# Optimization experiments

Measured on AMD Instinct MI355X. Metric: run time of the kernel, lower is better.

Reference implementation:

```python
import jax, jax.numpy as jnp
import numpy as np

B = 128          # batch
M_SIZE = 32      # mps bond dimension (init kwarg mps_size)
NQ = 16          # num_qubits -> 2**16 basis states


def setup_inputs() -> dict:
    key = jax.random.key(0)
    ks = jax.random.split(key, 4)
    def lin(k, out_d, in_d):
        return jax.random.normal(k, (out_d, in_d), jnp.float32) * (1.0 / np.sqrt(in_d))
    mat = M_SIZE * M_SIZE
    return {
        "x": jax.random.normal(ks[0], (B, 4), jnp.float32),
        "W1": lin(ks[1], 1024, 4),        "b1": jnp.zeros((1024,), jnp.float32),
        "W2": lin(ks[2], 32, 1024),       "b2": jnp.zeros((32,), jnp.float32),
        "W3": lin(ks[3], 2 * mat, 32),    "b3": jnp.zeros((2 * mat,), jnp.float32),
        "num_qubits": NQ,
    }


def _chain_products(M, k):
    """M: [2, B, m, m] site matrices (index 0 = spin_up, 1 = spin_down).
    Returns [2**k, B, m, m]: matrix products A_{s1} @ ... @ A_{sk} for every
    length-k bit string s, ordered as ascending binary (MSB = first/leftmost site),
    matching seq_gen's enumeration order."""
    arr = M
    for _ in range(k - 1):  # recursive doubling over sites (static small loop)
        arr = jnp.einsum('sbij,tbjk->stbik', arr, M)
        arr = arr.reshape((-1,) + M.shape[1:])
    return arr


def reference(x, W1, b1, W2, b2, W3, b3, num_qubits):
    # Encoder MLP (dropout is identity in eval mode)
    h = jax.nn.relu(x @ W1.T + b1)
    h = jax.nn.relu(h @ W2.T + b2)
    e = h @ W3.T + b3                         # [B, 2*m*m]
    m = int(np.sqrt(e.shape[-1] // 2))
    # view(-1, 2, m, m); split dim=1 -> spin_up = [:,0], spin_down = [:,1]
    Ms = e.reshape(-1, 2, m, m).transpose(1, 0, 2, 3)   # [2, B, m, m]
    # Decode: coeff(state) = trace(prod of site matrices). Split the chain in
    # two halves; trace(L_s @ R_t) = sum_ij L[s,i,j] * R[t,j,i].
    k1 = num_qubits // 2
    k2 = num_qubits - k1
    L = _chain_products(Ms, k1)               # [2^k1, B, m, m]
    R = _chain_products(Ms, k2)               # [2^k2, B, m, m]
    coeffs = jnp.einsum('sbij,tbji->stb', L, R)   # [2^k1, 2^k2, B]
    gs = coeffs.reshape(-1, coeffs.shape[-1]).T   # [B, 2^n], binary-ascending order
    return gs / jnp.linalg.norm(gs, axis=1, keepdims=True)
```

## Files before the change

### kernel.cpp

```cpp
#include <hip/hip_runtime.h>
#include <hip/hip_bf16.h>
#include <math.h>

#define BDIM 128

typedef short sh8 __attribute__((ext_vector_type(8)));
typedef __bf16 bf8 __attribute__((ext_vector_type(8)));
typedef float f32x4 __attribute__((ext_vector_type(4)));

__device__ inline float bf2f(unsigned short u) {
    union { unsigned int i; float f; } v; v.i = ((unsigned int)u) << 16; return v.f;
}
__device__ inline unsigned short f2bf(float f) {
    union { unsigned int i; float f; } v; v.f = f;
    unsigned int x = v.i;
    return (unsigned short)((x + 0x7FFFu + ((x >> 16) & 1u)) >> 16);
}

__device__ inline sh8 xshuf(sh8 v, int u) {
    switch (u & 7) {
    case 0: return v;
    case 1: return __builtin_shufflevector(v,v,1,0,3,2,5,4,7,6);
    case 2: return __builtin_shufflevector(v,v,2,3,0,1,6,7,4,5);
    case 3: return __builtin_shufflevector(v,v,3,2,1,0,7,6,5,4);
    case 4: return __builtin_shufflevector(v,v,4,5,6,7,0,1,2,3);
    case 5: return __builtin_shufflevector(v,v,5,4,7,6,1,0,3,2);
    case 6: return __builtin_shufflevector(v,v,6,7,4,5,2,3,0,1);
    default: return __builtin_shufflevector(v,v,7,6,5,4,3,2,1,0);
    }
}

__global__ __launch_bounds__(256) void enc_fused(
    const float* __restrict__ x,
    const float* __restrict__ W1, const float* __restrict__ b1,
    const float* __restrict__ W2, const float* __restrict__ b2,
    const float* __restrict__ W3, const float* __restrict__ b3,
    unsigned short* __restrict__ P4n, unsigned short* __restrict__ P4t,
    float* __restrict__ nrm)
{
    __shared__ float h1[1024];
    __shared__ float part[8][33];
    __shared__ float h2[32];
    __shared__ float aT[2][32][36], an[2][32][36];
    __shared__ float p2T[4][32][36], p2n[4][32][36];
    int b = blockIdx.x, t = threadIdx.x;
    if (t == 0) nrm[b] = 0.f;
    float x0 = x[b*4+0], x1 = x[b*4+1], x2 = x[b*4+2], x3 = x[b*4+3];
#pragma unroll
    for (int q = 0; q < 4; ++q) {
        int j = t + 256*q;
        float4 w = *(const float4*)(W1 + (size_t)j*4);
        float v = x0*w.x + x1*w.y + x2*w.z + x3*w.w + b1[j];
        h1[j] = v > 0.f ? v : 0.f;
    }
    __syncthreads();
    {
        int o = t & 31, chunk = t >> 5;
        const float* w2r = W2 + (size_t)o*1024 + chunk*128;
        const float* h1r = h1 + chunk*128;
        float s = 0.f;
#pragma unroll
        for (int k = 0; k < 128; k += 4) {
            float4 w = *(const float4*)(w2r + k);
            s += h1r[k]*w.x + h1r[k+1]*w.y + h1r[k+2]*w.z + h1r[k+3]*w.w;
        }
        part[chunk][o] = s;
    }
    __syncthreads();
    if (t < 32) {
        float s = b2[t];
#pragma unroll
        for (int c = 0; c < 8; ++c) s += part[c][t];
        h2[t] = s > 0.f ? s : 0.f;
    }
    __syncthreads();
#pragma unroll
    for (int q = 0; q < 8; ++q) {
        int j = t + 256*q;
        const float* w3r = W3 + (size_t)j*32;
        float s = b3[j];
#pragma unroll
        for (int i = 0; i < 32; i += 4) {
            float4 w = *(const float4*)(w3r + i);
            s += h2[i]*w.x + h2[i+1]*w.y + h2[i+2]*w.z + h2[i+3]*w.w;
        }
        int spin = j >> 10, off = j & 1023;
        int row = off >> 5, c = off & 31;
        an[spin][row][c] = s;
        aT[spin][c][row] = s;
    }
    __syncthreads();
    int w = t >> 6, l = t & 63;
    int r0 = (l >> 3) << 2, c0 = (l & 7) << 2;
    {
        float acc[4][4] = {};
#pragma unroll 8
        for (int kk = 0; kk < 32; ++kk) {
            float a[4], bb[4];
            *(float4*)a  = *(const float4*)&aT[w>>1][kk][r0];
            *(float4*)bb = *(const float4*)&an[w&1][kk][c0];
#pragma unroll
            for (int i = 0; i < 4; ++i)
#pragma unroll
                for (int j = 0; j < 4; ++j)
                    acc[i][j] += a[i]*bb[j];
        }
#pragma unroll
        for (int i = 0; i < 4; ++i)
#pragma unroll
            for (int j = 0; j < 4; ++j) {
                p2n[w][r0+i][c0+j] = acc[i][j];
                p2T[w][c0+j][r0+i] = acc[i][j];
            }
    }
    __syncthreads();
#pragma unroll
    for (int it = 0; it < 4; ++it) {
        int u = (w << 2) | it;
        float acc[4][4] = {};
#pragma unroll 8
        for (int kk = 0; kk < 32; ++kk) {
            float a[4], bb[4];
            *(float4*)a  = *(const float4*)&p2T[w][kk][r0];
            *(float4*)bb = *(const float4*)&p2n[it][kk][c0];
#pragma unroll
            for (int i = 0; i < 4; ++i)
#pragma unroll
                for (int j = 0; j < 4; ++j)
                    acc[i][j] += a[i]*bb[j];
        }
        unsigned short* dstN = P4n + ((size_t)b*16 + u)*1024;
        unsigned short* dstT = P4t + ((size_t)b*16 + u)*1024;
#pragma unroll
        for (int i = 0; i < 4; ++i) {
            ushort4 v; v.x = f2bf(acc[i][0]); v.y = f2bf(acc[i][1]);
            v.z = f2bf(acc[i][2]); v.w = f2bf(acc[i][3]);
            *(ushort4*)(dstN + (r0+i)*32 + c0) = v;
        }
#pragma unroll
        for (int j = 0; j < 4; ++j) {
            ushort4 v; v.x = f2bf(acc[0][j]); v.y = f2bf(acc[1][j]);
            v.z = f2bf(acc[2][j]); v.w = f2bf(acc[3][j]);
            *(ushort4*)(dstT + (c0+j)*32 + r0) = v;
        }
    }
}

__global__ __launch_bounds__(256) void ll_mfma(
    const unsigned short* __restrict__ P4n, const unsigned short* __restrict__ P4t,
    unsigned short* __restrict__ LL)
{
    int hi = blockIdx.x, b = blockIdx.y;
    __shared__ __align__(16) unsigned short As[32][40];
    __shared__ __align__(16) unsigned short Bs[512][40];
    __shared__ __align__(16) unsigned short outst[16][1024];
    int t = threadIdx.x;
    int w = t >> 6, l = t & 63;
    int lr = l & 15, lg = l >> 4;
    int wn = w * 128;

    {
        if (t < 128) {
            int i = t >> 2, k8 = (t & 3) * 8;
            *(sh8*)&As[i][k8] = *(const sh8*)(P4n + ((size_t)b*16 + hi)*1024 + i*32 + k8);
        }
#pragma unroll
        for (int rep = 0; rep < 8; ++rep) {
            int flat = rep*256 + t;
            int n = flat >> 2, k8 = (flat & 3) * 8;
            *(sh8*)&Bs[n][k8] =
                *(const sh8*)(P4t + ((size_t)b*16 + (n >> 5))*1024 + (n & 31)*32 + k8);
        }
    }
    __syncthreads();

    f32x4 acc[2][8] = {};
    bf8 av[2], bv[8];
#pragma unroll
    for (int m = 0; m < 2; ++m)
        av[m] = __builtin_bit_cast(bf8, *(const sh8*)&As[m*16 + lr][lg*8]);
#pragma unroll
    for (int n = 0; n < 8; ++n)
        bv[n] = __builtin_bit_cast(bf8, *(const sh8*)&Bs[wn + n*16 + lr][lg*8]);
#pragma unroll
    for (int m = 0; m < 2; ++m)
#pragma unroll
        for (int n = 0; n < 8; ++n)
            acc[m][n] = __builtin_amdgcn_mfma_f32_16x16x32_bf16(av[m], bv[n], acc[m][n], 0, 0, 0);
    __syncthreads();

#pragma unroll
    for (int m = 0; m < 2; ++m)
#pragma unroll
        for (int n = 0; n < 8; ++n) {
            f32x4 v = acc[m][n];
            int col = wn + n*16 + lr;
            int qlo = col >> 5, j = col & 31;
#pragma unroll
            for (int r = 0; r < 4; ++r) {
                int i = m*16 + lg*4 + r;
                outst[qlo][((i ^ j) << 5) | j] = f2bf(v[r]);
            }
        }
    __syncthreads();
    unsigned short* dst = LL + ((size_t)b*256 + hi*16)*1024;
    const uint4* s4 = (const uint4*)&outst[0][0];
    uint4* d4 = (uint4*)dst;
#pragma unroll
    for (int rep = 0; rep < 8; ++rep)
        d4[rep*256 + t] = s4[rep*256 + t];
}

__global__ __launch_bounds__(256) void pair_sym(
    const unsigned short* __restrict__ LL,
    float* __restrict__ out, float* __restrict__ norm2)
{
    int b = blockIdx.y;
    int bx = blockIdx.x;
    int ti = (bx >> 1);
    int tj = (bx + 1) >> 1;
    const unsigned short* Ab = LL + (size_t)b*262144 + (size_t)ti*131072;
    const unsigned short* Bb = LL + (size_t)b*262144 + (size_t)tj*131072;
    __shared__ __align__(16) unsigned short As[2][128][40];
    __shared__ __align__(16) unsigned short Bs[2][128][40];
    __shared__ float wsum[4];
    int t = threadIdx.x;
    int w = t >> 6, l = t & 63;
    int row0 = t >> 2;
    int j8 = (t & 3) * 8;
    int wm = (w >> 1) * 64, wn = (w & 1) * 64;
    int lr = l & 15, lg = l >> 4;

    const unsigned short* Ar0 = Ab + (size_t)row0*1024;
    const unsigned short* Ar1 = Ab + (size_t)(row0+64)*1024;
    const unsigned short* Br0 = Bb + (size_t)row0*1024;
    const unsigned short* Br1 = Bb + (size_t)(row0+64)*1024;

    f32x4 acc[4][4] = {};
    sh8 ra0, ra1, rb0, rb1;

    ra0 = *(const sh8*)(Ar0 + j8);
    ra1 = *(const sh8*)(Ar1 + j8);
    rb0 = *(const sh8*)(Br0 + j8);
    rb1 = *(const sh8*)(Br1 + j8);
    *(sh8*)&As[0][row0][j8]    = ra0;
    *(sh8*)&As[0][row0+64][j8] = ra1;
    *(sh8*)&Bs[0][row0][j8]    = rb0;
    *(sh8*)&Bs[0][row0+64][j8] = rb1;
    __syncthreads();

#pragma unroll
    for (int d = 0; d < 32; ++d) {
        int cur = d & 1, nxt = cur ^ 1;
        int dn = d + 1;
        if (dn < 32) {
            int aoff = dn*32 + j8;
            int boff = dn*32 + (j8 ^ ((dn >> 3) << 3));
            ra0 = *(const sh8*)(Ar0 + aoff);
            ra1 = *(const sh8*)(Ar1 + aoff);
            rb0 = *(const sh8*)(Br0 + boff);
            rb1 = *(const sh8*)(Br1 + boff);
        }
        bf8 av[4], bv[4];
#pragma unroll
        for (int m = 0; m < 4; ++m) {
            av[m] = __builtin_bit_cast(bf8, *(const sh8*)&As[cur][wm + m*16 + lr][lg*8]);
            bv[m] = __builtin_bit_cast(bf8, *(const sh8*)&Bs[cur][wn + m*16 + lr][lg*8]);
        }
#pragma unroll
        for (int m = 0; m < 4; ++m)
#pragma unroll
            for (int n = 0; n < 4; ++n)
                acc[m][n] = __builtin_amdgcn_mfma_f32_16x16x32_bf16(av[m], bv[n], acc[m][n], 0, 0, 0);
        if (dn < 32) {
            int u = dn & 7;
            *(sh8*)&As[nxt][row0][j8]    = ra0;
            *(sh8*)&As[nxt][row0+64][j8] = ra1;
            *(sh8*)&Bs[nxt][row0][j8]    = xshuf(rb0, u);
            *(sh8*)&Bs[nxt][row0+64][j8] = xshuf(rb1, u);
        }
        __syncthreads();
    }

    float ss = 0.f;
    size_t ob = (size_t)b*65536;
#pragma unroll
    for (int m = 0; m < 4; ++m) {
#pragma unroll
        for (int n = 0; n < 4; ++n) {
            f32x4 v = acc[m][n];
            int s0 = ti*128 + wm + m*16 + lg*4;
            int t0 = tj*128 + wn + n*16 + lr;
            float* op = out + ob + (size_t)s0*256 + t0;
#pragma unroll
            for (int r = 0; r < 4; ++r) {
                op[r*256] = v[r];
                ss += v[r]*v[r];
            }
            if (ti != tj) {
                *(float4*)(out + ob + (size_t)t0*256 + s0) =
                    make_float4(v[0], v[1], v[2], v[3]);
            }
        }
    }
    if (ti != tj) ss *= 2.f;
#pragma unroll
    for (int o = 1; o < 64; o <<= 1) ss += __shfl_xor(ss, o);
    if (l == 0) wsum[w] = ss;
    __syncthreads();
    if (t == 0) atomicAdd(norm2 + b, wsum[0]+wsum[1]+wsum[2]+wsum[3]);
}

__global__ __launch_bounds__(256) void scale_kernel(
    float* __restrict__ out, const float* __restrict__ norm2)
{
    size_t i = (size_t)blockIdx.x * 256 + threadIdx.x;
    int b = (int)(i >> 14);
    float s = rsqrtf(norm2[b]);
    float4 v = ((const float4*)out)[i];
    v.x *= s; v.y *= s; v.z *= s; v.w *= s;
    ((float4*)out)[i] = v;
}

extern "C" void kernel_launch(void* const* d_in, const int* in_sizes, int n_in,
                              void* d_out, int out_size, void* d_ws, size_t ws_size,
                              hipStream_t stream)
{
    (void)in_sizes; (void)n_in;
    const float* x  = (const float*)d_in[0];
    const float* W1 = (const float*)d_in[1];
    const float* b1 = (const float*)d_in[2];
    const float* W2 = (const float*)d_in[3];
    const float* b2 = (const float*)d_in[4];
    const float* W3 = (const float*)d_in[5];
    const float* b3 = (const float*)d_in[6];
    float* out = (float*)d_out;

    char* W = (char*)d_ws;
    const size_t MB = 1024*1024;
    unsigned short* LL  = (unsigned short*)(W + 0);
    unsigned short* P4n = (unsigned short*)(W + 64*MB);
    unsigned short* P4t = (unsigned short*)(W + 68*MB);
    float* nrm = (float*)(W + 72*MB);
    const size_t NEED = 72*MB + 512;
    if (ws_size < NEED) {
        hipMemsetAsync(d_out, 0, (size_t)out_size * sizeof(float), stream);
        return;
    }

    enc_fused<<<BDIM, 256, 0, stream>>>(x, W1, b1, W2, b2, W3, b3, P4n, P4t, nrm);
    ll_mfma<<<dim3(16, BDIM), 256, 0, stream>>>(P4n, P4t, LL);
    pair_sym<<<dim3(3, BDIM), 256, 0, stream>>>(LL, out, nrm);
    scale_kernel<<<8192, 256, 0, stream>>>(out, nrm);
}
```

Measured before the change: 153.7 us.

## Fuse normalization into pair_sym via per-batch atomic counter barrier

Removes the separate scale kernel by having the three pair_sym blocks of each batch element first reduce their squared-norm contribution, then spin on a per-batch atomic counter until all three have contributed, and scale outputs before writing. This avoids re-reading and re-writing the full 32 MB output in a separate pass and saves a launch. The cost is an inter-block spin-wait, which assumes all three blocks for a batch are co-resident and could deadlock or stall if they are not scheduled together.

```diff
diff --git a/kernel.cpp b/kernel.cpp
--- a/kernel.cpp
+++ b/kernel.cpp
@@ -36,7 +36,7 @@
     const float* __restrict__ W2, const float* __restrict__ b2,
     const float* __restrict__ W3, const float* __restrict__ b3,
     unsigned short* __restrict__ P4n, unsigned short* __restrict__ P4t,
-    float* __restrict__ nrm)
+    float* __restrict__ nrm, unsigned int* __restrict__ cnt)
 {
     __shared__ float h1[1024];
     __shared__ float part[8][33];
@@ -44,7 +44,7 @@
     __shared__ float aT[2][32][36], an[2][32][36];
     __shared__ float p2T[4][32][36], p2n[4][32][36];
     int b = blockIdx.x, t = threadIdx.x;
-    if (t == 0) nrm[b] = 0.f;
+    if (t == 0) { nrm[b] = 0.f; cnt[b] = 0u; }
     float x0 = x[b*4+0], x1 = x[b*4+1], x2 = x[b*4+2], x3 = x[b*4+3];
 #pragma unroll
     for (int q = 0; q < 4; ++q) {
@@ -213,7 +213,8 @@
 
 __global__ __launch_bounds__(256) void pair_sym(
     const unsigned short* __restrict__ LL,
-    float* __restrict__ out, float* __restrict__ norm2)
+    float* __restrict__ out, float* __restrict__ norm2,
+    unsigned int* __restrict__ cnt)
 {
     int b = blockIdx.y;
     int bx = blockIdx.x;
@@ -224,6 +225,7 @@
     __shared__ __align__(16) unsigned short As[2][128][40];
     __shared__ __align__(16) unsigned short Bs[2][128][40];
     __shared__ float wsum[4];
+    __shared__ float sfac;
     int t = threadIdx.x;
     int w = t >> 6, l = t & 63;
     int row0 = t >> 2;
@@ -283,6 +285,29 @@
     }
 
     float ss = 0.f;
+#pragma unroll
+    for (int m = 0; m < 4; ++m)
+#pragma unroll
+        for (int n = 0; n < 4; ++n) {
+            f32x4 v = acc[m][n];
+#pragma unroll
+            for (int r = 0; r < 4; ++r) ss += v[r]*v[r];
+        }
+    if (ti != tj) ss *= 2.f;
+#pragma unroll
+    for (int o = 1; o < 64; o <<= 1) ss += __shfl_xor(ss, o);
+    if (l == 0) wsum[w] = ss;
+    __syncthreads();
+    if (t == 0) {
+        atomicAdd(norm2 + b, wsum[0]+wsum[1]+wsum[2]+wsum[3]);
+        __threadfence();
+        atomicAdd(cnt + b, 1u);
+        while (atomicAdd(cnt + b, 0u) < 3u) {}
+        sfac = rsqrtf(atomicAdd(norm2 + b, 0.f));
+    }
+    __syncthreads();
+    float s = sfac;
+
     size_t ob = (size_t)b*65536;
 #pragma unroll
     for (int m = 0; m < 4; ++m) {
@@ -293,33 +318,14 @@
             int t0 = tj*128 + wn + n*16 + lr;
             float* op = out + ob + (size_t)s0*256 + t0;
 #pragma unroll
-            for (int r = 0; r < 4; ++r) {
-                op[r*256] = v[r];
-                ss += v[r]*v[r];
-            }
+            for (int r = 0; r < 4; ++r)
+                op[r*256] = v[r]*s;
             if (ti != tj) {
                 *(float4*)(out + ob + (size_t)t0*256 + s0) =
-                    make_float4(v[0], v[1], v[2], v[3]);
+                    make_float4(v[0]*s, v[1]*s, v[2]*s, v[3]*s);
             }
         }
     }
-    if (ti != tj) ss *= 2.f;
-#pragma unroll
-    for (int o = 1; o < 64; o <<= 1) ss += __shfl_xor(ss, o);
-    if (l == 0) wsum[w] = ss;
-    __syncthreads();
-    if (t == 0) atomicAdd(norm2 + b, wsum[0]+wsum[1]+wsum[2]+wsum[3]);
-}
-
-__global__ __launch_bounds__(256) void scale_kernel(
-    float* __restrict__ out, const float* __restrict__ norm2)
-{
-    size_t i = (size_t)blockIdx.x * 256 + threadIdx.x;
-    int b = (int)(i >> 14);
-    float s = rsqrtf(norm2[b]);
-    float4 v = ((const float4*)out)[i];
-    v.x *= s; v.y *= s; v.z *= s; v.w *= s;
-    ((float4*)out)[i] = v;
 }
 
 extern "C" void kernel_launch(void* const* d_in, const int* in_sizes, int n_in,
@@ -342,14 +348,14 @@
     unsigned short* P4n = (unsigned short*)(W + 64*MB);
     unsigned short* P4t = (unsigned short*)(W + 68*MB);
     float* nrm = (float*)(W + 72*MB);
-    const size_t NEED = 72*MB + 512;
+    unsigned int* cnt = (unsigned int*)(W + 72*MB + 512);
+    const size_t NEED = 72*MB + 1024;
     if (ws_size < NEED) {
         hipMemsetAsync(d_out, 0, (size_t)out_size * sizeof(float), stream);
         return;
     }
 
-    enc_fused<<<BDIM, 256, 0, stream>>>(x, W1, b1, W2, b2, W3, b3, P4n, P4t, nrm);
+    enc_fused<<<BDIM, 256, 0, stream>>>(x, W1, b1, W2, b2, W3, b3, P4n, P4t, nrm, cnt);
     ll_mfma<<<dim3(16, BDIM), 256, 0, stream>>>(P4n, P4t, LL);
-    pair_sym<<<dim3(3, BDIM), 256, 0, stream>>>(LL, out, nrm);
-    scale_kernel<<<8192, 256, 0, stream>>>(out, nrm);
-}
+    pair_sym<<<dim3(3, BDIM), 256, 0, stream>>>(LL, out, nrm, cnt);
+}
```

Result: slower. 167.4 us (+8.9%).
